# Optimization experiments

Hardware: AMD Instinct MI355X
Metric: run time of the kernel (lower is better)

The kernel has to match this reference:

```python
import jax, jax.numpy as jnp
import numpy as np

D_MODEL = 1024
N_HEAD = 16
N_BR = 4
DH = D_MODEL // N_HEAD            # 64
H_TOT = N_BR * N_HEAD             # 64
SCALE = float(np.pi / np.sqrt(3.0))
ATTN_SCALE = DH ** -0.5


def _rope(x):
    # x: (B, H, T, Dh). Non-interleaved variant: output is cat of the two rotated halves.
    B, H, T, Dh = x.shape
    inv_freq = 1.0 / (10000.0 ** (jnp.arange(0, Dh, 2, dtype=jnp.float32) / Dh))  # (Dh/2,)
    t = jnp.arange(T, dtype=jnp.float32)
    freqs = t[:, None] * inv_freq[None, :]        # (T, Dh/2)
    cos = jnp.cos(freqs)[None, None]              # (1,1,T,Dh/2)
    sin = jnp.sin(freqs)[None, None]
    x1 = x[..., 0::2]
    x2 = x[..., 1::2]
    return jnp.concatenate([-x2 * sin + x1 * cos, x1 * sin + x2 * cos], axis=-1)


def setup_inputs() -> dict:
    key = jax.random.key(0)
    ks = jax.random.split(key, 8)
    s = 0.02
    B, T = 1, 1024
    return {
        "X": jax.random.normal(ks[0], (B, T, D_MODEL), jnp.float32),
        "Wq": jax.random.normal(ks[1], (D_MODEL, H_TOT * DH), jnp.float32) * s,
        "bq": jnp.zeros((H_TOT * DH,), jnp.float32),
        "Wk": jax.random.normal(ks[2], (D_MODEL, D_MODEL), jnp.float32) * s,
        "bk": jnp.zeros((D_MODEL,), jnp.float32),
        "Wv": jax.random.normal(ks[3], (D_MODEL, H_TOT * DH), jnp.float32) * s,
        "bv": jnp.zeros((H_TOT * DH,), jnp.float32),
        "sink_scalars": jax.random.normal(ks[4], (H_TOT, 1, 1), jnp.float32) * s,
        "v_nulls": jax.random.normal(ks[5], (H_TOT, DH), jnp.float32) * s,
        "Wo": jax.random.normal(ks[6], (D_MODEL, D_MODEL), jnp.float32) * s,
        "bo": jnp.zeros((D_MODEL,), jnp.float32),
    }


def reference(X, Wq, bq, Wk, bk, Wv, bv, sink_scalars, v_nulls, Wo, bo):
    B, T, C = X.shape
    q = (X @ Wq + bq).reshape(B, T, H_TOT, DH).transpose(0, 2, 1, 3)   # (B,H,T,Dh)
    v = (X @ Wv + bv).reshape(B, T, H_TOT, DH).transpose(0, 2, 1, 3)
    k_base = (X @ Wk + bk).reshape(B, T, N_HEAD, DH).transpose(0, 2, 1, 3)  # (B,Nh,T,Dh)
    k = jnp.tile(k_base, (1, N_BR, 1, 1))                               # (B,H,T,Dh)

    q = _rope(q)
    k = _rope(k)

    scores = jnp.einsum('bhtd,bhsd->bhts', q, k) * ATTN_SCALE           # (B,H,T,T)
    key_self = jnp.clip(jnp.sum(k * k, axis=-1), 1e-6, None)            # (B,H,T)
    denom = jnp.sqrt(key_self)[:, :, None, :]                           # (B,H,1,T)
    w = jax.nn.softplus(scores / denom)

    causal = jnp.tril(jnp.ones((T, T), dtype=bool))                     # keep lower triangle
    w = jnp.where(causal[None, None], w, 0.0)
    w = w * jax.nn.sigmoid(SCALE * w)

    sinks = jnp.tanh(sink_scalars).reshape(1, H_TOT, 1, 1) + 1e-6       # (1,H,1,1)
    alpha = 1.0 / (jnp.sum(w, axis=-1, keepdims=True) + sinks + 1e-6)   # (B,H,T,1)
    probs_tokens = w * alpha
    probs_sink = sinks * alpha                                          # (B,H,T,1)

    out_tokens = jnp.einsum('bhts,bhsd->bhtd', probs_tokens, v)
    out_sinks = probs_sink * v_nulls[None, :, None, :]                  # (B,H,T,Dh)
    context = out_tokens + out_sinks                                    # (B,H,T,Dh)

    context = context.reshape(B, N_BR, N_HEAD, T, DH)
    context = context.transpose(0, 1, 3, 2, 4).reshape(B, N_BR, T, C)
    y = context @ Wo + bo                                               # (B,N_BR,T,C)
    return jnp.mean(y, axis=1)


if __name__ == "__main__":
    out = reference(**setup_inputs())
    print(out.shape)
```

## Files before the change

kernel.cpp:

```cpp
#include <hip/hip_runtime.h>
#include <math.h>

#define SILU_SCALE 1.8137993642342178f
#define QKV_N 9216
#define LN2 0.6931471805599453f
#define DNSCALE 0.18033688011112042f

typedef __attribute__((ext_vector_type(8))) short bf16x8;
typedef __attribute__((ext_vector_type(4))) float f32x4;

#if __has_builtin(__builtin_amdgcn_exp2f)
#define EXP2(x) __builtin_amdgcn_exp2f(x)
#else
#define EXP2(x) exp2f(x)
#endif
#if __has_builtin(__builtin_amdgcn_logf)
#define LOG2(x) __builtin_amdgcn_logf(x)
#else
#define LOG2(x) __log2f(x)
#endif

__device__ __forceinline__ unsigned short f2bf(float f){
    union { float f; unsigned int i; } u; u.f = f;
    unsigned int r = u.i + 0x7FFFu + ((u.i >> 16) & 1u);
    return (unsigned short)(r >> 16);
}
__device__ __forceinline__ float bf2f(unsigned short s){
    union { unsigned int i; float f; } u; u.i = ((unsigned int)s) << 16;
    return u.f;
}
__device__ __forceinline__ unsigned int pack_bf2(float lo, float hi){
    unsigned int i0 = __float_as_uint(lo) + 0x8000u;
    unsigned int i1 = __float_as_uint(hi) + 0x8000u;
    return __builtin_amdgcn_perm(i1, i0, 0x07060302u);
}

__device__ __forceinline__ void gload_lds16(const void* g, void* l){
    __builtin_amdgcn_global_load_lds(
        (const __attribute__((address_space(1))) void*)g,
        (__attribute__((address_space(3))) void*)l, 16, 0, 0);
}

__global__ __launch_bounds__(256) void prep_kernel(
    const float* __restrict__ X,
    const float* __restrict__ Wq, const float* __restrict__ Wk,
    const float* __restrict__ Wv, const float* __restrict__ Wo,
    const float* __restrict__ bq, const float* __restrict__ bk,
    const float* __restrict__ bv,
    unsigned short* __restrict__ Xb, unsigned short* __restrict__ WqkvT,
    unsigned short* __restrict__ WoT, float* __restrict__ qkvb)
{
    __shared__ float t[32][33];
    int b = blockIdx.x;
    const int tid = threadIdx.x;

    if (b >= 10240){
        if (b < 10752){
            int i = ((b - 10240) * 256 + tid) * 8;
            float4 a = *(const float4*)&X[i];
            float4 c = *(const float4*)&X[i + 4];
            union { unsigned short u[8]; uint4 v; } o;
            o.u[0]=f2bf(a.x); o.u[1]=f2bf(a.y); o.u[2]=f2bf(a.z); o.u[3]=f2bf(a.w);
            o.u[4]=f2bf(c.x); o.u[5]=f2bf(c.y); o.u[6]=f2bf(c.z); o.u[7]=f2bf(c.w);
            *(uint4*)&Xb[i] = o.v;
        } else {
            int i = (b - 10752) * 256 + tid;
            float v;
            if (i < 4096) v = bq[i];
            else if (i < 5120) v = bk[i - 4096];
            else v = bv[i - 5120];
            qkvb[i] = v;
        }
        return;
    }

    const float* W; unsigned short* Wt; int N, tiles_x;
    if (b < 4096)      { W = Wq; Wt = WqkvT;                       N = 4096; tiles_x = 128; }
    else if (b < 5120) { b -= 4096; W = Wk; Wt = WqkvT + (size_t)4096*1024; N = 1024; tiles_x = 32; }
    else if (b < 9216) { b -= 5120; W = Wv; Wt = WqkvT + (size_t)5120*1024; N = 4096; tiles_x = 128; }
    else               { b -= 9216; W = Wo; Wt = WoT;              N = 1024; tiles_x = 32; }

    const int k0 = (b / tiles_x) * 32, n0 = (b % tiles_x) * 32;
    const int r = tid >> 3, c4 = (tid & 7) * 4;
    float4 v = *(const float4*)&W[(size_t)(k0 + r) * N + n0 + c4];
    t[c4+0][r] = v.x; t[c4+1][r] = v.y; t[c4+2][r] = v.z; t[c4+3][r] = v.w;
    __syncthreads();
    union { unsigned short u[4]; uint2 v; } o;
    o.u[0]=f2bf(t[r][c4+0]); o.u[1]=f2bf(t[r][c4+1]);
    o.u[2]=f2bf(t[r][c4+2]); o.u[3]=f2bf(t[r][c4+3]);
    *(uint2*)&Wt[(size_t)(n0 + r) * 1024 + k0 + c4] = o.v;
}

template<int BM, int BN, int OUTBF>
__global__ __launch_bounds__(256) void gemm_k(
    const unsigned short* __restrict__ A,
    const unsigned short* __restrict__ Bt,
    const float* __restrict__ bias,
    void* __restrict__ Cout, int M, int N, int K)
{
    constexpr int MT = BM / 32;
    constexpr int NT = BN / 32;
    __shared__ unsigned short As[BM * 64];
    __shared__ unsigned short Bs[BN * 64];
    const int tid  = threadIdx.x;
    const int wave = tid >> 6;
    const int lane = tid & 63;
    const int l15  = lane & 15;
    const int quad = lane >> 4;
    const int m0 = blockIdx.y * BM;
    const int n0 = blockIdx.x * BN;
    const int wm = (wave >> 1) * (BM / 2);
    const int wn = (wave & 1) * (BN / 2);

    f32x4 acc[MT][NT];
    #pragma unroll
    for (int i = 0; i < MT; i++)
        #pragma unroll
        for (int j = 0; j < NT; j++)
            acc[i][j] = (f32x4){0.f, 0.f, 0.f, 0.f};

    for (int k0 = 0; k0 < K; k0 += 64){
        #pragma unroll
        for (int j = 0; j < (BM * 8) / 256; j++){
            int bslot = j * 256 + wave * 64;
            int slot = bslot + lane;
            int row = slot >> 3, phys = slot & 7;
            int c = phys ^ (row & 7);
            gload_lds16(&A[(size_t)(m0 + row) * K + k0 + c * 8], &As[bslot * 8]);
        }
        #pragma unroll
        for (int j = 0; j < (BN * 8) / 256; j++){
            int bslot = j * 256 + wave * 64;
            int slot = bslot + lane;
            int row = slot >> 3, phys = slot & 7;
            int c = phys ^ (row & 7);
            gload_lds16(&Bt[(size_t)(n0 + row) * K + k0 + c * 8], &Bs[bslot * 8]);
        }
        __syncthreads();
        #pragma unroll
        for (int ks = 0; ks < 2; ks++){
            bf16x8 af[MT], bfr[NT];
            #pragma unroll
            for (int i = 0; i < MT; i++){
                int row = wm + i * 16 + l15;
                int phys = (ks * 4 + quad) ^ (row & 7);
                af[i] = *(const bf16x8*)&As[row * 64 + phys * 8];
            }
            #pragma unroll
            for (int j = 0; j < NT; j++){
                int row = wn + j * 16 + l15;
                int phys = (ks * 4 + quad) ^ (row & 7);
                bfr[j] = *(const bf16x8*)&Bs[row * 64 + phys * 8];
            }
            #pragma unroll
            for (int i = 0; i < MT; i++)
                #pragma unroll
                for (int j = 0; j < NT; j++)
                    acc[i][j] = __builtin_amdgcn_mfma_f32_16x16x32_bf16(af[i], bfr[j], acc[i][j], 0, 0, 0);
        }
        __syncthreads();
    }
    #pragma unroll
    for (int i = 0; i < MT; i++){
        #pragma unroll
        for (int j = 0; j < NT; j++){
            int col = n0 + wn + j * 16 + l15;
            float bv = bias[col];
            #pragma unroll
            for (int r = 0; r < 4; r++){
                int row = m0 + wm + i * 16 + quad * 4 + r;
                float v = acc[i][j][r] + bv;
                if (OUTBF) ((unsigned short*)Cout)[(size_t)row * N + col] = f2bf(v);
                else       ((float*)Cout)[(size_t)row * N + col] = v;
            }
        }
    }
}

__global__ void rope_kernel(unsigned short* __restrict__ qkv, float* __restrict__ dninv)
{
    int idx = blockIdx.x * blockDim.x + threadIdx.x;
    if (idx < 65536){
        int t = idx >> 6, h = idx & 63;
        unsigned short* p = qkv + (size_t)t * QKV_N + h * 64;
        uint4 raw[8];
        #pragma unroll
        for (int i = 0; i < 8; i++) raw[i] = *(const uint4*)(p + i * 8);
        const unsigned short* rp = (const unsigned short*)raw;
        float x[64];
        #pragma unroll
        for (int i = 0; i < 64; i++) x[i] = bf2f(rp[i]);
        unsigned short o[64];
        #pragma unroll
        for (int d = 0; d < 32; d++){
            float inv = EXP2(-(float)d * 0.4152410118609203f);
            float s, c; __sincosf((float)t * inv, &s, &c);
            float x1 = x[2*d], x2 = x[2*d+1];
            o[d]      = f2bf(x1 * c - x2 * s);
            o[d + 32] = f2bf(x1 * s + x2 * c);
        }
        #pragma unroll
        for (int i = 0; i < 8; i++) *(uint4*)(p + i * 8) = ((const uint4*)o)[i];
    } else {
        idx -= 65536;
        int t = idx >> 4, h = idx & 15;
        unsigned short* p = qkv + (size_t)t * QKV_N + 4096 + h * 64;
        uint4 raw[8];
        #pragma unroll
        for (int i = 0; i < 8; i++) raw[i] = *(const uint4*)(p + i * 8);
        const unsigned short* rp = (const unsigned short*)raw;
        float x[64];
        #pragma unroll
        for (int i = 0; i < 64; i++) x[i] = bf2f(rp[i]);
        unsigned short o[64];
        float ss = 0.f;
        #pragma unroll
        for (int d = 0; d < 32; d++){
            float inv = EXP2(-(float)d * 0.4152410118609203f);
            float s, c; __sincosf((float)t * inv, &s, &c);
            float x1 = x[2*d], x2 = x[2*d+1];
            float a = x1 * c - x2 * s;
            float b = x1 * s + x2 * c;
            ss = fmaf(a, a, fmaf(b, b, ss));
            o[d]      = f2bf(a);
            o[d + 32] = f2bf(b);
        }
        #pragma unroll
        for (int i = 0; i < 8; i++) *(uint4*)(p + i * 8) = ((const uint4*)o)[i];
        dninv[h * 1024 + t] = DNSCALE * rsqrtf(fmaxf(ss, 1e-6f));
    }
}

__global__ __launch_bounds__(512) void attn_mfma(
    const unsigned short* __restrict__ qkv,
    const float* __restrict__ dninv,
    const float* __restrict__ sinks, const float* __restrict__ vnulls,
    unsigned short* __restrict__ ctx)
{
    __shared__ unsigned short ks[64 * 64];
    __shared__ unsigned short vt[64 * 64];
    __shared__ unsigned short ws[2][64][72];
    __shared__ float dl[64];
    __shared__ float dsum[8][16];

    const int tid  = threadIdx.x;
    const int wave = tid >> 6;
    const int tile = wave >> 2;
    const int w    = wave & 3;
    const int lane = tid & 63;
    const int l15  = lane & 15;
    const int quad = lane >> 4;
    const int h  = blockIdx.y;
    const int kh = h & 15;
    const int pi = blockIdx.x;
    const int qtB = 15 - pi;
    const int qt  = tile ? qtB : pi;
    const int t0  = qt << 6;

    const unsigned short* Q  = qkv;
    const unsigned short* Kp = qkv + 4096;
    const unsigned short* V  = qkv + 5120;

    bf16x8 qf0, qf1;
    {
        const unsigned short* qp = Q + (size_t)(t0 + w * 16 + l15) * QKV_N + h * 64;
        qf0 = *(const bf16x8*)(qp + quad * 8);
        qf1 = *(const bf16x8*)(qp + 32 + quad * 8);
    }

    f32x4 acc_o[4];
    #pragma unroll
    for (int i = 0; i < 4; i++) acc_o[i] = (f32x4){0.f, 0.f, 0.f, 0.f};
    float den = 0.f;
    const int q_glob = t0 + w * 16 + l15;

    const int pr  = (tid & 255) >> 3;
    const int cch = tid & 7;

    for (int st = 0; st <= qtB; st++){
        const int s0 = st << 6;
        __syncthreads();

        {
            int bslot = wave * 64;
            int slot = bslot + lane;
            int row = slot >> 3, phys = slot & 7;
            int c = phys ^ (row & 7);
            gload_lds16(&Kp[(size_t)(s0 + row) * QKV_N + kh * 64 + c * 8], &ks[bslot * 8]);
        }
        if (tid < 256){
            uint4 g0 = *(const uint4*)&V[(size_t)(s0 + 2 * pr)     * QKV_N + h * 64 + cch * 8];
            uint4 g1 = *(const uint4*)&V[(size_t)(s0 + 2 * pr + 1) * QKV_N + h * 64 + cch * 8];
            const unsigned short* p0 = (const unsigned short*)&g0;
            const unsigned short* p1 = (const unsigned short*)&g1;
            #pragma unroll
            for (int j = 0; j < 8; j++){
                int d = cch * 8 + j;
                int physc = (pr >> 2) ^ ((d ^ (d >> 3)) & 7);
                unsigned int val = (unsigned int)p0[j] | ((unsigned int)p1[j] << 16);
                ((unsigned int*)vt)[d * 32 + physc * 4 + (pr & 3)] = val;
            }
        } else if (tid < 320){
            dl[tid - 256] = dninv[kh * 1024 + s0 + (tid - 256)];
        }
        __syncthreads();

        if (st > qt) continue;
        const bool diag = (st == qt);

        #pragma unroll
        for (int nt = 0; nt < 4; nt++){
            const int sbase = nt * 16 + quad * 4;
            uint2* wp = (uint2*)&ws[tile][w * 16 + l15][sbase];
            if (diag && nt > w){ *wp = (uint2){0u, 0u}; continue; }

            f32x4 sc = (f32x4){0.f, 0.f, 0.f, 0.f};
            {
                int srow = nt * 16 + l15;
                int ph0 = quad ^ (srow & 7);
                int ph1 = (4 + quad) ^ (srow & 7);
                bf16x8 kf0 = *(const bf16x8*)&ks[srow * 64 + ph0 * 8];
                bf16x8 kf1 = *(const bf16x8*)&ks[srow * 64 + ph1 * 8];
                sc = __builtin_amdgcn_mfma_f32_16x16x32_bf16(kf0, qf0, sc, 0, 0, 0);
                sc = __builtin_amdgcn_mfma_f32_16x16x32_bf16(kf1, qf1, sc, 0, 0, 0);
            }
            float da[4];
            *(float4*)da = *(const float4*)&dl[sbase];
            float w4[4];
            #pragma unroll
            for (int r = 0; r < 4; r++){
                float y = sc[r] * da[r];
                float p = EXP2(-fabsf(y));
                float u = fmaxf(y, 0.f) + LOG2(1.f + p);
                float e3 = EXP2(-SILU_SCALE * u);
                float wv = __fdividef(LN2 * u, 1.f + e3);
                wv = (s0 + sbase + r <= q_glob) ? wv : 0.f;
                den += wv;
                w4[r] = wv;
            }
            uint2 pk;
            pk.x = pack_bf2(w4[0], w4[1]);
            pk.y = pack_bf2(w4[2], w4[3]);
            *wp = pk;
        }

        {
            const int prow = w * 16 + l15;
            bf16x8 pf0 = *(const bf16x8*)&ws[tile][prow][quad * 8];
            bf16x8 pf1 = *(const bf16x8*)&ws[tile][prow][32 + quad * 8];
            const bool skip_hi = diag && (w <= 1);
            #pragma unroll
            for (int dt = 0; dt < 4; dt++){
                int d = dt * 16 + l15;
                int swz = (d ^ (d >> 3)) & 7;
                bf16x8 vf0 = *(const bf16x8*)&vt[d * 64 + (quad ^ swz) * 8];
                acc_o[dt] = __builtin_amdgcn_mfma_f32_16x16x32_bf16(pf0, vf0, acc_o[dt], 0, 0, 0);
                if (!skip_hi){
                    bf16x8 vf1 = *(const bf16x8*)&vt[d * 64 + ((4 + quad) ^ swz) * 8];
                    acc_o[dt] = __builtin_amdgcn_mfma_f32_16x16x32_bf16(pf1, vf1, acc_o[dt], 0, 0, 0);
                }
            }
        }
    }

    den += __shfl_xor(den, 16);
    den += __shfl_xor(den, 32);
    if (quad == 0) dsum[wave][l15] = den;
    float den4[4];
    *(float4*)den4 = *(const float4*)&dsum[wave][quad * 4];

    float sinkv = tanhf(sinks[h]) + 1e-6f;
    #pragma unroll
    for (int r = 0; r < 4; r++){
        int qg = t0 + w * 16 + quad * 4 + r;
        float alpha = __fdividef(1.f, den4[r] + sinkv + 1e-6f);
        #pragma unroll
        for (int dt = 0; dt < 4; dt++){
            int d = dt * 16 + l15;
            float o = (acc_o[dt][r] + sinkv * vnulls[h * 64 + d]) * alpha;
            ctx[((size_t)h * 1024 + qg) * 64 + d] = f2bf(o);
        }
    }
}

__global__ void avg_kernel(const unsigned short* __restrict__ ctx, unsigned short* __restrict__ avg)
{
    int i8 = (blockIdx.x * 256 + threadIdx.x) * 8;
    int t = i8 >> 10, c = i8 & 1023;
    int nh = c >> 6, d = c & 63;
    float s[8] = {};
    #pragma unroll
    for (int br = 0; br < 4; br++){
        uint4 v = *(const uint4*)&ctx[((size_t)(br * 16 + nh) * 1024 + t) * 64 + d];
        const unsigned short* p = (const unsigned short*)&v;
        #pragma unroll
        for (int j = 0; j < 8; j++) s[j] += bf2f(p[j]);
    }
    union { unsigned short u[8]; uint4 v; } o;
    #pragma unroll
    for (int j = 0; j < 8; j++) o.u[j] = f2bf(0.25f * s[j]);
    *(uint4*)&avg[i8] = o.v;
}

extern "C" void kernel_launch(void* const* d_in, const int* in_sizes, int n_in,
                              void* d_out, int out_size, void* d_ws, size_t ws_size,
                              hipStream_t stream)
{
    (void)in_sizes; (void)n_in; (void)out_size; (void)ws_size;
    const float* X      = (const float*)d_in[0];
    const float* Wq     = (const float*)d_in[1];
    const float* bq     = (const float*)d_in[2];
    const float* Wk     = (const float*)d_in[3];
    const float* bk     = (const float*)d_in[4];
    const float* Wv     = (const float*)d_in[5];
    const float* bv     = (const float*)d_in[6];
    const float* sinks  = (const float*)d_in[7];
    const float* vnulls = (const float*)d_in[8];
    const float* Wo     = (const float*)d_in[9];
    const float* bo     = (const float*)d_in[10];
    float* out = (float*)d_out;

    unsigned short* w16   = (unsigned short*)d_ws;
    unsigned short* Xb    = w16;
    unsigned short* WqkvT = Xb    + (size_t)1024 * 1024;
    unsigned short* QKVb  = WqkvT + (size_t)QKV_N * 1024;
    unsigned short* WoT   = QKVb  + (size_t)1024 * QKV_N;
    unsigned short* ctxb  = WoT   + (size_t)1024 * 1024;
    unsigned short* avgb  = ctxb  + (size_t)64 * 1024 * 64;
    float* qkvb = (float*)(avgb + (size_t)1024 * 1024);
    float* dnf  = qkvb + QKV_N;

    dim3 blk(256);
    prep_kernel<<<10788, blk, 0, stream>>>(X, Wq, Wk, Wv, Wo, bq, bk, bv,
                                           Xb, WqkvT, WoT, qkvb);
    gemm_k<128, 96, 1><<<dim3(96, 8), blk, 0, stream>>>(Xb, WqkvT, qkvb, QKVb, 1024, QKV_N, 1024);
    rope_kernel<<<320, blk, 0, stream>>>(QKVb, dnf);
    attn_mfma<<<dim3(8, 64), dim3(512), 0, stream>>>(QKVb, dnf, sinks, vnulls, ctxb);
    avg_kernel<<<512, blk, 0, stream>>>(ctxb, avgb);
    gemm_k<64, 64, 0><<<dim3(16, 16), blk, 0, stream>>>(avgb, WoT, bo, out, 1024, 1024, 1024);
}
```

Measured before the change: 212.9 us.

## Use 64x64 transpose tiles in prep and split-K the output projection GEMM

The weight transpose/convert kernel now processes 64x64 tiles per block with 16-byte bf16 stores, cutting the block count and widening the writes. The final Wo GEMM is replaced by a 2-way split-K kernel with 128x64 tiles that writes fp32 partials into the reused WqkvT workspace, followed by a reduce kernel that adds the partials and the bias. The aim is cheaper prep traffic and more blocks for the small output GEMM, at the cost of an extra launch and extra partial-sum memory traffic.

```diff
diff --git a/kernel.cpp b/kernel.cpp
--- a/kernel.cpp
+++ b/kernel.cpp
@@ -50,13 +50,13 @@
     unsigned short* __restrict__ Xb, unsigned short* __restrict__ WqkvT,
     unsigned short* __restrict__ WoT, float* __restrict__ qkvb)
 {
-    __shared__ float t[32][33];
+    __shared__ float t[64][65];
     int b = blockIdx.x;
     const int tid = threadIdx.x;
 
-    if (b >= 10240){
-        if (b < 10752){
-            int i = ((b - 10240) * 256 + tid) * 8;
+    if (b >= 2560){
+        if (b < 3072){
+            int i = ((b - 2560) * 256 + tid) * 8;
             float4 a = *(const float4*)&X[i];
             float4 c = *(const float4*)&X[i + 4];
             union { unsigned short u[8]; uint4 v; } o;
@@ -64,7 +64,7 @@
             o.u[4]=f2bf(c.x); o.u[5]=f2bf(c.y); o.u[6]=f2bf(c.z); o.u[7]=f2bf(c.w);
             *(uint4*)&Xb[i] = o.v;
         } else {
-            int i = (b - 10752) * 256 + tid;
+            int i = (b - 3072) * 256 + tid;
             float v;
             if (i < 4096) v = bq[i];
             else if (i < 5120) v = bk[i - 4096];
@@ -75,20 +75,32 @@
     }
 
     const float* W; unsigned short* Wt; int N, tiles_x;
-    if (b < 4096)      { W = Wq; Wt = WqkvT;                       N = 4096; tiles_x = 128; }
-    else if (b < 5120) { b -= 4096; W = Wk; Wt = WqkvT + (size_t)4096*1024; N = 1024; tiles_x = 32; }
-    else if (b < 9216) { b -= 5120; W = Wv; Wt = WqkvT + (size_t)5120*1024; N = 4096; tiles_x = 128; }
-    else               { b -= 9216; W = Wo; Wt = WoT;              N = 1024; tiles_x = 32; }
-
-    const int k0 = (b / tiles_x) * 32, n0 = (b % tiles_x) * 32;
-    const int r = tid >> 3, c4 = (tid & 7) * 4;
-    float4 v = *(const float4*)&W[(size_t)(k0 + r) * N + n0 + c4];
-    t[c4+0][r] = v.x; t[c4+1][r] = v.y; t[c4+2][r] = v.z; t[c4+3][r] = v.w;
+    if (b < 1024)      { W = Wq; Wt = WqkvT;                       N = 4096; tiles_x = 64; }
+    else if (b < 1280) { b -= 1024; W = Wk; Wt = WqkvT + (size_t)4096*1024; N = 1024; tiles_x = 16; }
+    else if (b < 2304) { b -= 1280; W = Wv; Wt = WqkvT + (size_t)5120*1024; N = 4096; tiles_x = 64; }
+    else               { b -= 2304; W = Wo; Wt = WoT;              N = 1024; tiles_x = 16; }
+
+    const int k0 = (b / tiles_x) * 64, n0 = (b % tiles_x) * 64;
+    const int lr  = tid >> 4;
+    const int lc4 = (tid & 15) * 4;
+    #pragma unroll
+    for (int p = 0; p < 4; p++){
+        int r = lr + p * 16;
+        float4 v = *(const float4*)&W[(size_t)(k0 + r) * N + n0 + lc4];
+        t[lc4+0][r] = v.x; t[lc4+1][r] = v.y;
+        t[lc4+2][r] = v.z; t[lc4+3][r] = v.w;
+    }
     __syncthreads();
-    union { unsigned short u[4]; uint2 v; } o;
-    o.u[0]=f2bf(t[r][c4+0]); o.u[1]=f2bf(t[r][c4+1]);
-    o.u[2]=f2bf(t[r][c4+2]); o.u[3]=f2bf(t[r][c4+3]);
-    *(uint2*)&Wt[(size_t)(n0 + r) * 1024 + k0 + c4] = o.v;
+    const int wr  = tid >> 3;
+    const int wc8 = (tid & 7) * 8;
+    #pragma unroll
+    for (int p = 0; p < 2; p++){
+        int r = wr + p * 32;
+        union { unsigned short u[8]; uint4 v; } o;
+        #pragma unroll
+        for (int j = 0; j < 8; j++) o.u[j] = f2bf(t[r][wc8 + j]);
+        *(uint4*)&Wt[(size_t)(n0 + r) * 1024 + k0 + wc8] = o.v;
+    }
 }
 
 template<int BM, int BN, int OUTBF>
@@ -177,6 +189,102 @@
     }
 }
 
+__global__ __launch_bounds__(256) void gemm_wo(
+    const unsigned short* __restrict__ A,
+    const unsigned short* __restrict__ Bt,
+    float* __restrict__ P)
+{
+    constexpr int BM = 128, BN = 64, MT = 4, NT = 2;
+    __shared__ unsigned short As[BM * 64];
+    __shared__ unsigned short Bs[BN * 64];
+    const int tid  = threadIdx.x;
+    const int wave = tid >> 6;
+    const int lane = tid & 63;
+    const int l15  = lane & 15;
+    const int quad = lane >> 4;
+    const int m0 = blockIdx.y * BM;
+    const int n0 = blockIdx.x * BN;
+    const int kz = blockIdx.z;
+    const int wm = (wave >> 1) * 64;
+    const int wn = (wave & 1) * 32;
+
+    f32x4 acc[MT][NT];
+    #pragma unroll
+    for (int i = 0; i < MT; i++)
+        #pragma unroll
+        for (int j = 0; j < NT; j++)
+            acc[i][j] = (f32x4){0.f, 0.f, 0.f, 0.f};
+
+    const int kbeg = kz * 512;
+    for (int k0 = kbeg; k0 < kbeg + 512; k0 += 64){
+        #pragma unroll
+        for (int j = 0; j < (BM * 8) / 256; j++){
+            int bslot = j * 256 + wave * 64;
+            int slot = bslot + lane;
+            int row = slot >> 3, phys = slot & 7;
+            int c = phys ^ (row & 7);
+            gload_lds16(&A[(size_t)(m0 + row) * 1024 + k0 + c * 8], &As[bslot * 8]);
+        }
+        #pragma unroll
+        for (int j = 0; j < (BN * 8) / 256; j++){
+            int bslot = j * 256 + wave * 64;
+            int slot = bslot + lane;
+            int row = slot >> 3, phys = slot & 7;
+            int c = phys ^ (row & 7);
+            gload_lds16(&Bt[(size_t)(n0 + row) * 1024 + k0 + c * 8], &Bs[bslot * 8]);
+        }
+        __syncthreads();
+        #pragma unroll
+        for (int ks = 0; ks < 2; ks++){
+            bf16x8 af[MT], bfr[NT];
+            #pragma unroll
+            for (int i = 0; i < MT; i++){
+                int row = wm + i * 16 + l15;
+                int phys = (ks * 4 + quad) ^ (row & 7);
+                af[i] = *(const bf16x8*)&As[row * 64 + phys * 8];
+            }
+            #pragma unroll
+            for (int j = 0; j < NT; j++){
+                int row = wn + j * 16 + l15;
+                int phys = (ks * 4 + quad) ^ (row & 7);
+                bfr[j] = *(const bf16x8*)&Bs[row * 64 + phys * 8];
+            }
+            #pragma unroll
+            for (int i = 0; i < MT; i++)
+                #pragma unroll
+                for (int j = 0; j < NT; j++)
+                    acc[i][j] = __builtin_amdgcn_mfma_f32_16x16x32_bf16(af[i], bfr[j], acc[i][j], 0, 0, 0);
+        }
+        __syncthreads();
+    }
+    float* Pz = P + (size_t)kz * 1024 * 1024;
+    #pragma unroll
+    for (int i = 0; i < MT; i++){
+        #pragma unroll
+        for (int j = 0; j < NT; j++){
+            int col = n0 + wn + j * 16 + l15;
+            #pragma unroll
+            for (int r = 0; r < 4; r++){
+                int row = m0 + wm + i * 16 + quad * 4 + r;
+                Pz[(size_t)row * 1024 + col] = acc[i][j][r];
+            }
+        }
+    }
+}
+
+__global__ void wo_reduce(const float* __restrict__ P, const float* __restrict__ bo,
+                          float* __restrict__ out)
+{
+    int i = (blockIdx.x * 256 + threadIdx.x) * 4;
+    float4 a = *(const float4*)&P[i];
+    float4 b = *(const float4*)&P[1024 * 1024 + i];
+    float4 c = *(const float4*)&bo[i & 1023];
+    float4 o;
+    o.x = a.x + b.x + c.x; o.y = a.y + b.y + c.y;
+    o.z = a.z + b.z + c.z; o.w = a.w + b.w + c.w;
+    *(float4*)&out[i] = o;
+}
+
 __global__ void rope_kernel(unsigned short* __restrict__ qkv, float* __restrict__ dninv)
 {
     int idx = blockIdx.x * blockDim.x + threadIdx.x;
@@ -429,13 +537,15 @@
     unsigned short* avgb  = ctxb  + (size_t)64 * 1024 * 64;
     float* qkvb = (float*)(avgb + (size_t)1024 * 1024);
     float* dnf  = qkvb + QKV_N;
+    float* pWo  = (float*)WqkvT;
 
     dim3 blk(256);
-    prep_kernel<<<10788, blk, 0, stream>>>(X, Wq, Wk, Wv, Wo, bq, bk, bv,
-                                           Xb, WqkvT, WoT, qkvb);
+    prep_kernel<<<3108, blk, 0, stream>>>(X, Wq, Wk, Wv, Wo, bq, bk, bv,
+                                          Xb, WqkvT, WoT, qkvb);
     gemm_k<128, 96, 1><<<dim3(96, 8), blk, 0, stream>>>(Xb, WqkvT, qkvb, QKVb, 1024, QKV_N, 1024);
     rope_kernel<<<320, blk, 0, stream>>>(QKVb, dnf);
     attn_mfma<<<dim3(8, 64), dim3(512), 0, stream>>>(QKVb, dnf, sinks, vnulls, ctxb);
     avg_kernel<<<512, blk, 0, stream>>>(ctxb, avgb);
-    gemm_k<64, 64, 0><<<dim3(16, 16), blk, 0, stream>>>(avgb, WoT, bo, out, 1024, 1024, 1024);
-}
+    gemm_wo<<<dim3(16, 8, 2), blk, 0, stream>>>(avgb, WoT, pWo);
+    wo_reduce<<<1024, blk, 0, stream>>>(pWo, bo, out);
+}
```

Measured after the change: 209.2 us. No clear change (-1.7%).
